# Performance work log

Measured on AMD Instinct MI355X. Metric: run time of the kernel, lower is better.

Reference implementation:

```python
import math
import jax, jax.numpy as jnp
import numpy as np

DIM = 1024
HEADS = 16
KV_HEADS = 4            # use_mqa: heads // 4
HEAD_DIM = DIM // HEADS  # 64
KV_DIM = KV_HEADS * HEAD_DIM  # 256
WINDOW = 64
SCALE = HEAD_DIM ** -0.5


def _alibi_slopes(n_heads: int) -> np.ndarray:
    # n_heads is a power of 2 here
    start = 2.0 ** (-(2.0 ** (-(math.log2(n_heads) - 3))))
    return np.array([start * (start ** i) for i in range(n_heads)], dtype=np.float32)


def setup_inputs() -> dict:
    key = jax.random.key(0)
    ks = jax.random.split(key, 5)
    B, N = 1, 2048
    x = jax.random.normal(ks[0], (B, N, DIM), dtype=jnp.float32)
    # Linear weights stored as [in, out] (applied as x @ W)
    sq = 1.0 / math.sqrt(DIM)
    Wq = jax.random.uniform(ks[1], (DIM, DIM), jnp.float32, -sq, sq)
    Wk = jax.random.uniform(ks[2], (DIM, KV_DIM), jnp.float32, -sq, sq)
    Wv = jax.random.uniform(ks[3], (DIM, KV_DIM), jnp.float32, -sq, sq)
    Wo = jax.random.uniform(ks[4], (DIM, DIM), jnp.float32, -sq, sq)
    return {"x": x, "Wq": Wq, "Wk": Wk, "Wv": Wv, "Wo": Wo}


def reference(x, Wq, Wk, Wv, Wo):
    B, N, C = x.shape
    # projections -> [B, H, N, hd]
    q = (x @ Wq).reshape(B, N, HEADS, HEAD_DIM).transpose(0, 2, 1, 3)
    k = (x @ Wk).reshape(B, N, KV_HEADS, HEAD_DIM).transpose(0, 2, 1, 3)
    v = (x @ Wv).reshape(B, N, KV_HEADS, HEAD_DIM).transpose(0, 2, 1, 3)
    # MQA: repeat kv heads (torch repeat_interleave on head dim)
    rep = HEADS // KV_HEADS
    k = jnp.repeat(k, rep, axis=1)
    v = jnp.repeat(v, rep, axis=1)

    scores = jnp.einsum("bhqd,bhkd->bhqk", q, k) * SCALE  # [B,H,N,N]

    # ALiBi bias: distance[i, j] = j - i, scaled per head
    idx = jnp.arange(N)
    dist = (idx[None, :] - idx[:, None]).astype(scores.dtype)  # [N, N]
    slopes = jnp.asarray(_alibi_slopes(HEADS))                 # [H]
    scores = scores + dist[None, None, :, :] * slopes[None, :, None, None]

    # causal AND local band (|i-j| <= WINDOW) -> allowed iff j in [i-WINDOW, i]
    causal = idx[None, :] <= idx[:, None]
    band = jnp.abs(idx[:, None] - idx[None, :]) <= WINDOW
    allowed = causal & band  # [N, N]
    scores_local = jnp.where(allowed[None, None], scores, -jnp.inf)
    attn_local = jax.nn.softmax(scores_local, axis=-1)
    out_local = jnp.einsum("bhqk,bhkd->bhqd", attn_local, v)

    # global: strided keys every WINDOW positions, full (non-causal) softmax
    k_g = k[:, :, ::WINDOW, :]
    v_g = v[:, :, ::WINDOW, :]
    scores_g = jnp.einsum("bhqd,bhkd->bhqk", q, k_g) * SCALE
    attn_g = jax.nn.softmax(scores_g, axis=-1)
    out_global = jnp.einsum("bhqk,bhkd->bhqd", attn_g, v_g)

    out = (out_local + out_global).transpose(0, 2, 1, 3).reshape(B, N, C)
    return out @ Wo
```

## Files before the change

kernel.cpp:

```cpp
#include <hip/hip_runtime.h>

#define SCALE 0.125f

typedef unsigned short ushort_t;
typedef unsigned short ushortx8 __attribute__((ext_vector_type(8)));
typedef unsigned short ushortx4 __attribute__((ext_vector_type(4)));
typedef short bf16x8 __attribute__((ext_vector_type(8)));
typedef float f32x4 __attribute__((ext_vector_type(4)));

__device__ inline ushort_t f2bf(float f) {
  unsigned int u = __float_as_uint(f);
  u += 0x7FFFu + ((u >> 16) & 1u);
  return (ushort_t)(u >> 16);
}
__device__ inline float bf2f(ushort_t u) {
  return __uint_as_float(((unsigned int)u) << 16);
}

__global__ __launch_bounds__(256) void prep_kernel(
    const float* __restrict__ x, const float* __restrict__ Wq, const float* __restrict__ Wk,
    const float* __restrict__ Wv, const float* __restrict__ Wo,
    ushort_t* __restrict__ x_bf, ushort_t* __restrict__ wqkv_t, ushort_t* __restrict__ wo_t)
{
  __shared__ float t[64][65];
  int bid = blockIdx.x;
  const int tid = threadIdx.x;
  if (bid < 2048) {
    int idx = (bid * 256 + tid) * 4;
    if (idx < 2048 * 1024) {
      float4 f = *(const float4*)(x + idx);
      ushortx4 o = { f2bf(f.x), f2bf(f.y), f2bf(f.z), f2bf(f.w) };
      *(ushortx4*)(x_bf + idx) = o;
    }
    return;
  }
  bid -= 2048;
  const float* src; int C; ushort_t* dst; int row_off, cb, kb;
  if (bid < 256)      { src = Wq; C = 1024; dst = wqkv_t; row_off = 0;    cb = bid & 15; kb = bid >> 4; }
  else if (bid < 320) { int j = bid - 256; src = Wk; C = 256; dst = wqkv_t; row_off = 1024; cb = j & 3; kb = j >> 2; }
  else if (bid < 384) { int j = bid - 320; src = Wv; C = 256; dst = wqkv_t; row_off = 1280; cb = j & 3; kb = j >> 2; }
  else                { int j = bid - 384; src = Wo; C = 1024; dst = wo_t; row_off = 0;    cb = j & 15; kb = j >> 4; }
  const int c0 = cb * 64, k0 = kb * 64;
  const int c = tid & 63, r4 = tid >> 6;
  for (int rr = r4; rr < 64; rr += 4)
    t[c][rr] = src[(size_t)(k0 + rr) * C + c0 + c];
  __syncthreads();
  const int kk = tid & 63, n4 = tid >> 6;
  for (int nn = n4; nn < 64; nn += 4)
    dst[(size_t)(row_off + c0 + nn) * 1024 + k0 + kk] = f2bf(t[nn][kk]);
}

__global__ __launch_bounds__(256) void gemm128_kernel(
    const ushort_t* __restrict__ A, const ushort_t* __restrict__ Bt, int mode, int ntn,
    ushort_t* __restrict__ qout, ushort_t* __restrict__ kout, ushort_t* __restrict__ vout,
    float* __restrict__ fout)
{
  __shared__ __align__(16) ushort_t lA[64 * 128];
  __shared__ __align__(16) ushort_t lB[64 * 128];
  const int bid = blockIdx.x;
  const int xcd = bid & 7, g = bid >> 3;
  const int m0 = (xcd + 8 * (g / ntn)) * 64;
  const int n0 = (g % ntn) * 64;

  const int tid = threadIdx.x;
  const int lane = tid & 63, w = tid >> 6;
  const int quad = lane >> 4, l16 = lane & 15;
  const int rw = (w >> 1) * 32, cw = (w & 1) * 32;

  const int rs = tid >> 4;
  const int ps = tid & 15;
  const int swz = ps ^ (rs & 15);
  const int eL = tid * 8;
  const ushort_t* Ab = A + (size_t)(m0 + rs) * 1024 + swz * 8;
  const ushort_t* Bb = Bt + (size_t)(n0 + rs) * 1024 + swz * 8;

  f32x4 acc[2][2] = {};

  for (int k0 = 0; k0 < 1024; k0 += 128) {
    __syncthreads();
#pragma unroll
    for (int rd = 0; rd < 4; ++rd) {
      __builtin_amdgcn_global_load_lds(
          (const __attribute__((address_space(1))) unsigned int*)(Ab + (size_t)rd * 16 * 1024 + k0),
          (__attribute__((address_space(3))) unsigned int*)(lA + eL + rd * 2048), 16, 0, 0);
      __builtin_amdgcn_global_load_lds(
          (const __attribute__((address_space(1))) unsigned int*)(Bb + (size_t)rd * 16 * 1024 + k0),
          (__attribute__((address_space(3))) unsigned int*)(lB + eL + rd * 2048), 16, 0, 0);
    }
    __syncthreads();

#pragma unroll
    for (int kh = 0; kh < 4; ++kh) {
      const int ca = ((kh * 4 + quad) ^ l16) << 3;
      bf16x8 a0 = *(const bf16x8*)(lA + (rw + l16) * 128      + ca);
      bf16x8 a1 = *(const bf16x8*)(lA + (rw + 16 + l16) * 128 + ca);
      bf16x8 b0 = *(const bf16x8*)(lB + (cw + l16) * 128      + ca);
      bf16x8 b1 = *(const bf16x8*)(lB + (cw + 16 + l16) * 128 + ca);
      acc[0][0] = __builtin_amdgcn_mfma_f32_16x16x32_bf16(a0, b0, acc[0][0], 0, 0, 0);
      acc[0][1] = __builtin_amdgcn_mfma_f32_16x16x32_bf16(a0, b1, acc[0][1], 0, 0, 0);
      acc[1][0] = __builtin_amdgcn_mfma_f32_16x16x32_bf16(a1, b0, acc[1][0], 0, 0, 0);
      acc[1][1] = __builtin_amdgcn_mfma_f32_16x16x32_bf16(a1, b1, acc[1][1], 0, 0, 0);
    }
  }

#pragma unroll
  for (int mg = 0; mg < 2; ++mg)
#pragma unroll
    for (int ng = 0; ng < 2; ++ng)
#pragma unroll
      for (int r = 0; r < 4; ++r) {
        const int row = m0 + rw + mg * 16 + quad * 4 + r;
        const int col = n0 + cw + ng * 16 + l16;
        const float v = acc[mg][ng][r];
        if (mode == 0) {
          if (n0 < 1024)       qout[(size_t)row * 1024 + col] = f2bf(v);
          else if (n0 < 1280)  kout[(size_t)row * 256 + (col - 1024)] = f2bf(v);
          else                 vout[(size_t)row * 256 + (col - 1280)] = f2bf(v);
        } else {
          fout[(size_t)row * 1024 + col] = v;
        }
      }
}

__global__ __launch_bounds__(256) void attn_mfma_kernel(
    const ushort_t* __restrict__ Q, const ushort_t* __restrict__ Kb,
    const ushort_t* __restrict__ Vb, ushort_t* __restrict__ O)
{
  __shared__ __align__(16) ushort_t lK[128 * 64];
  __shared__ __align__(16) ushort_t lVt[64 * 128];
  __shared__ __align__(16) ushort_t lKg[32 * 64];
  __shared__ __align__(16) ushort_t lVtg[64 * 40];
  __shared__ __align__(16) ushort_t lP[64 * 128];
  __shared__ __align__(16) ushort_t lPg[64 * 40];

  const int h = blockIdx.x, qb = blockIdx.y;
  const int tid = threadIdx.x;
  const int kvcol = (h >> 2) * 64;
  const int kbase = qb * 64 - 64;

  for (int cidx = tid; cidx < 1024; cidx += 256) {
    const int key = cidx >> 3, ch = cidx & 7;
    const int kpos = kbase + key;
    ushortx8 kv = {0,0,0,0,0,0,0,0}, vv = {0,0,0,0,0,0,0,0};
    if (kpos >= 0) {
      kv = *(const ushortx8*)(Kb + (size_t)kpos * 256 + kvcol + ch * 8);
      vv = *(const ushortx8*)(Vb + (size_t)kpos * 256 + kvcol + ch * 8);
    }
    *(ushortx8*)(lK + key * 64 + ((ch ^ (key & 7)) << 3)) = kv;
    const int kc = key >> 3, ke = key & 7;
#pragma unroll
    for (int e = 0; e < 8; ++e) {
      int dim = ch * 8 + e;
      lVt[dim * 128 + ((kc ^ (dim & 7)) << 3) + ke] = vv[e];
    }
  }
  {
    const int gk = tid >> 3, ch = tid & 7;
    const int kpos = gk * 64;
    ushortx8 kv = *(const ushortx8*)(Kb + (size_t)kpos * 256 + kvcol + ch * 8);
    ushortx8 vv = *(const ushortx8*)(Vb + (size_t)kpos * 256 + kvcol + ch * 8);
    *(ushortx8*)(lKg + gk * 64 + ((ch ^ (gk & 7)) << 3)) = kv;
#pragma unroll
    for (int e = 0; e < 8; ++e) lVtg[(ch * 8 + e) * 40 + gk] = vv[e];
  }
  __syncthreads();

  const int lane = tid & 63, w = tid >> 6;
  const int quad = lane >> 4, l16 = lane & 15;
  const int l7 = l16 & 7;
  const float slope = exp2f(-0.5f * (float)(h + 1));

  const int qrow = qb * 64 + w * 16 + l16;
  const ushort_t* qptr = Q + (size_t)qrow * 1024 + h * 64 + quad * 8;
  const bf16x8 aq0 = *(const bf16x8*)(qptr);
  const bf16x8 aq1 = *(const bf16x8*)(qptr + 32);

  float s[8][4];
#pragma unroll
  for (int kt = 0; kt < 8; ++kt) {
    const int key = kt * 16 + l16;
    const bf16x8 b0 = *(const bf16x8*)(lK + key * 64 + ((quad ^ l7) << 3));
    const bf16x8 b1 = *(const bf16x8*)(lK + key * 64 + (((4 + quad) ^ l7) << 3));
    f32x4 acc = {0.f, 0.f, 0.f, 0.f};
    acc = __builtin_amdgcn_mfma_f32_16x16x32_bf16(aq0, b0, acc, 0, 0, 0);
    acc = __builtin_amdgcn_mfma_f32_16x16x32_bf16(aq1, b1, acc, 0, 0, 0);
    const int kpos = kbase + key;
#pragma unroll
    for (int r = 0; r < 4; ++r) {
      const int qp = qb * 64 + w * 16 + quad * 4 + r;
      const int d = kpos - qp;
      const bool ok = (d <= 0) && (d >= -64) && (kpos >= 0);
      s[kt][r] = ok ? acc[r] * SCALE + (float)d * slope : -1e30f;
    }
  }
  float mr[4] = {-1e30f, -1e30f, -1e30f, -1e30f};
#pragma unroll
  for (int kt = 0; kt < 8; ++kt)
#pragma unroll
    for (int r = 0; r < 4; ++r) mr[r] = fmaxf(mr[r], s[kt][r]);
#pragma unroll
  for (int r = 0; r < 4; ++r) {
    mr[r] = fmaxf(mr[r], __shfl_xor(mr[r], 1));
    mr[r] = fmaxf(mr[r], __shfl_xor(mr[r], 2));
    mr[r] = fmaxf(mr[r], __shfl_xor(mr[r], 4));
    mr[r] = fmaxf(mr[r], __shfl_xor(mr[r], 8));
  }
  float lr[4] = {0.f, 0.f, 0.f, 0.f};
#pragma unroll
  for (int kt = 0; kt < 8; ++kt)
#pragma unroll
    for (int r = 0; r < 4; ++r) { float p = __expf(s[kt][r] - mr[r]); s[kt][r] = p; lr[r] += p; }
#pragma unroll
  for (int r = 0; r < 4; ++r) {
    lr[r] += __shfl_xor(lr[r], 1);
    lr[r] += __shfl_xor(lr[r], 2);
    lr[r] += __shfl_xor(lr[r], 4);
    lr[r] += __shfl_xor(lr[r], 8);
    lr[r] = 1.f / lr[r];
  }
#pragma unroll
  for (int kt = 0; kt < 8; ++kt) {
    const int kc = kt * 2 + (l16 >> 3);
#pragma unroll
    for (int r = 0; r < 4; ++r) {
      const int qr = w * 16 + quad * 4 + r;
      lP[qr * 128 + ((kc ^ (qr & 7)) << 3) + l7] = f2bf(s[kt][r] * lr[r]);
    }
  }

  float sg[2][4];
#pragma unroll
  for (int g16 = 0; g16 < 2; ++g16) {
    const int key = g16 * 16 + l16;
    const bf16x8 b0 = *(const bf16x8*)(lKg + key * 64 + ((quad ^ l7) << 3));
    const bf16x8 b1 = *(const bf16x8*)(lKg + key * 64 + (((4 + quad) ^ l7) << 3));
    f32x4 acc = {0.f, 0.f, 0.f, 0.f};
    acc = __builtin_amdgcn_mfma_f32_16x16x32_bf16(aq0, b0, acc, 0, 0, 0);
    acc = __builtin_amdgcn_mfma_f32_16x16x32_bf16(aq1, b1, acc, 0, 0, 0);
#pragma unroll
    for (int r = 0; r < 4; ++r) sg[g16][r] = acc[r] * SCALE;
  }
  float mg[4], lg[4];
#pragma unroll
  for (int r = 0; r < 4; ++r) {
    mg[r] = fmaxf(sg[0][r], sg[1][r]);
    mg[r] = fmaxf(mg[r], __shfl_xor(mg[r], 1));
    mg[r] = fmaxf(mg[r], __shfl_xor(mg[r], 2));
    mg[r] = fmaxf(mg[r], __shfl_xor(mg[r], 4));
    mg[r] = fmaxf(mg[r], __shfl_xor(mg[r], 8));
  }
#pragma unroll
  for (int r = 0; r < 4; ++r) {
    float p0 = __expf(sg[0][r] - mg[r]);
    float p1 = __expf(sg[1][r] - mg[r]);
    sg[0][r] = p0; sg[1][r] = p1;
    lg[r] = p0 + p1;
    lg[r] += __shfl_xor(lg[r], 1);
    lg[r] += __shfl_xor(lg[r], 2);
    lg[r] += __shfl_xor(lg[r], 4);
    lg[r] += __shfl_xor(lg[r], 8);
    lg[r] = 1.f / lg[r];
  }
#pragma unroll
  for (int g16 = 0; g16 < 2; ++g16)
#pragma unroll
    for (int r = 0; r < 4; ++r) {
      const int qr = w * 16 + quad * 4 + r;
      lPg[qr * 40 + g16 * 16 + l16] = f2bf(sg[g16][r] * lg[r]);
    }

  f32x4 acco[4] = {};
  const int qA = w * 16 + l16;
#pragma unroll
  for (int kki = 0; kki < 4; ++kki) {
    const bf16x8 ap = *(const bf16x8*)(lP + qA * 128 + (((kki * 4 + quad) ^ l7) << 3));
#pragma unroll
    for (int nt = 0; nt < 4; ++nt) {
      const int dim = nt * 16 + l16;
      const bf16x8 bv = *(const bf16x8*)(lVt + dim * 128 + (((kki * 4 + quad) ^ l7) << 3));
      acco[nt] = __builtin_amdgcn_mfma_f32_16x16x32_bf16(ap, bv, acco[nt], 0, 0, 0);
    }
  }
  {
    const bf16x8 apg = *(const bf16x8*)(lPg + qA * 40 + quad * 8);
#pragma unroll
    for (int nt = 0; nt < 4; ++nt) {
      const bf16x8 bvg = *(const bf16x8*)(lVtg + (nt * 16 + l16) * 40 + quad * 8);
      acco[nt] = __builtin_amdgcn_mfma_f32_16x16x32_bf16(apg, bvg, acco[nt], 0, 0, 0);
    }
  }
#pragma unroll
  for (int nt = 0; nt < 4; ++nt)
#pragma unroll
    for (int r = 0; r < 4; ++r) {
      const int qp = qb * 64 + w * 16 + quad * 4 + r;
      O[(size_t)qp * 1024 + h * 64 + nt * 16 + l16] = f2bf(acco[nt][r]);
    }
}

extern "C" void kernel_launch(void* const* d_in, const int* in_sizes, int n_in,
                              void* d_out, int out_size, void* d_ws, size_t ws_size,
                              hipStream_t stream)
{
  const float* x  = (const float*)d_in[0];
  const float* Wq = (const float*)d_in[1];
  const float* Wk = (const float*)d_in[2];
  const float* Wv = (const float*)d_in[3];
  const float* Wo = (const float*)d_in[4];
  float* out = (float*)d_out;

  char* ws = (char*)d_ws;
  ushort_t* x_bf   = (ushort_t*)(ws);
  ushort_t* wqkv_t = (ushort_t*)(ws + (4ull  << 20));
  ushort_t* wo_t   = (ushort_t*)(ws + (7ull  << 20));
  ushort_t* q_bf   = (ushort_t*)(ws + (9ull  << 20));
  ushort_t* k_bf   = (ushort_t*)(ws + (13ull << 20));
  ushort_t* v_bf   = (ushort_t*)(ws + (14ull << 20));
  ushort_t* at_bf  = (ushort_t*)(ws + (15ull << 20));

  prep_kernel<<<2688, 256, 0, stream>>>(x, Wq, Wk, Wv, Wo, x_bf, wqkv_t, wo_t);
  gemm128_kernel<<<768, 256, 0, stream>>>(x_bf, wqkv_t, 0, 24, q_bf, k_bf, v_bf, nullptr);
  attn_mfma_kernel<<<dim3(16, 32), 256, 0, stream>>>(q_bf, k_bf, v_bf, at_bf);
  gemm128_kernel<<<512, 256, 0, stream>>>(at_bf, wo_t, 1, 16, nullptr, nullptr, nullptr, out);
}
```

Before: 106.6 us.

## Make GEMMs persistent with double-buffered LDS prefetch across output tiles

Replaces the one-tile-per-block GEMM with a persistent kernel of 256 blocks, where each block walks several 64x64 output tiles sharing the same A rows. LDS is double-buffered so the next k-slice (or the next tile's first slice) is issued via global_load_lds before computing the current one, removing one barrier per step. Launch overhead and tail waves go down and the A-tile stays hot in cache. The cost is fewer concurrent blocks (256 against the CU count), less latency hiding from occupancy, and twice the LDS per block.

```diff
diff --git a/kernel.cpp b/kernel.cpp
--- a/kernel.cpp
+++ b/kernel.cpp
@@ -50,76 +50,91 @@
     dst[(size_t)(row_off + c0 + nn) * 1024 + k0 + kk] = f2bf(t[nn][kk]);
 }
 
-__global__ __launch_bounds__(256) void gemm128_kernel(
-    const ushort_t* __restrict__ A, const ushort_t* __restrict__ Bt, int mode, int ntn,
+__global__ __launch_bounds__(256) void gemm_pers_kernel(
+    const ushort_t* __restrict__ A, const ushort_t* __restrict__ Bt, int mode, int tpb,
     ushort_t* __restrict__ qout, ushort_t* __restrict__ kout, ushort_t* __restrict__ vout,
     float* __restrict__ fout)
 {
-  __shared__ __align__(16) ushort_t lA[64 * 128];
-  __shared__ __align__(16) ushort_t lB[64 * 128];
+  __shared__ __align__(16) ushort_t lA[2 * 64 * 128];
+  __shared__ __align__(16) ushort_t lB[2 * 64 * 128];
   const int bid = blockIdx.x;
-  const int xcd = bid & 7, g = bid >> 3;
-  const int m0 = (xcd + 8 * (g / ntn)) * 64;
-  const int n0 = (g % ntn) * 64;
+  const int xcd = bid & 7, idx = bid >> 3;
+  const int m0 = (xcd * 4 + (idx & 3)) * 64;
+  const int n_base = idx >> 2;
 
   const int tid = threadIdx.x;
   const int lane = tid & 63, w = tid >> 6;
   const int quad = lane >> 4, l16 = lane & 15;
   const int rw = (w >> 1) * 32, cw = (w & 1) * 32;
 
-  const int rs = tid >> 4;
-  const int ps = tid & 15;
+  const int rs = tid >> 4, ps = tid & 15;
   const int swz = ps ^ (rs & 15);
   const int eL = tid * 8;
   const ushort_t* Ab = A + (size_t)(m0 + rs) * 1024 + swz * 8;
-  const ushort_t* Bb = Bt + (size_t)(n0 + rs) * 1024 + swz * 8;
-
+  const ushort_t* Bb0 = Bt + (size_t)(n_base * 64 + rs) * 1024 + swz * 8;
+
+  const int NS = tpb * 8;
   f32x4 acc[2][2] = {};
 
-  for (int k0 = 0; k0 < 1024; k0 += 128) {
+#define STAGE(s, b)                                                                             \
+  do {                                                                                          \
+    const int j_ = (s) >> 3, k0_ = ((s) & 7) * 128;                                             \
+    const ushort_t* Bb_ = Bb0 + (size_t)j_ * 512 * 1024;                                        \
+    const int off_ = (b) * 8192;                                                                \
+    _Pragma("unroll")                                                                           \
+    for (int rd = 0; rd < 4; ++rd) {                                                            \
+      __builtin_amdgcn_global_load_lds(                                                         \
+          (const __attribute__((address_space(1))) unsigned int*)(Ab + (size_t)rd * 16 * 1024 + k0_), \
+          (__attribute__((address_space(3))) unsigned int*)(lA + off_ + eL + rd * 2048), 16, 0, 0);   \
+      __builtin_amdgcn_global_load_lds(                                                         \
+          (const __attribute__((address_space(1))) unsigned int*)(Bb_ + (size_t)rd * 16 * 1024 + k0_), \
+          (__attribute__((address_space(3))) unsigned int*)(lB + off_ + eL + rd * 2048), 16, 0, 0);   \
+    }                                                                                           \
+  } while (0)
+
+  STAGE(0, 0);
+
+  for (int s = 0; s < NS; ++s) {
+    const int b = s & 1;
     __syncthreads();
-#pragma unroll
-    for (int rd = 0; rd < 4; ++rd) {
-      __builtin_amdgcn_global_load_lds(
-          (const __attribute__((address_space(1))) unsigned int*)(Ab + (size_t)rd * 16 * 1024 + k0),
-          (__attribute__((address_space(3))) unsigned int*)(lA + eL + rd * 2048), 16, 0, 0);
-      __builtin_amdgcn_global_load_lds(
-          (const __attribute__((address_space(1))) unsigned int*)(Bb + (size_t)rd * 16 * 1024 + k0),
-          (__attribute__((address_space(3))) unsigned int*)(lB + eL + rd * 2048), 16, 0, 0);
-    }
-    __syncthreads();
-
+    if (s + 1 < NS) STAGE(s + 1, b ^ 1);
+    const int off = b * 8192;
 #pragma unroll
     for (int kh = 0; kh < 4; ++kh) {
       const int ca = ((kh * 4 + quad) ^ l16) << 3;
-      bf16x8 a0 = *(const bf16x8*)(lA + (rw + l16) * 128      + ca);
-      bf16x8 a1 = *(const bf16x8*)(lA + (rw + 16 + l16) * 128 + ca);
-      bf16x8 b0 = *(const bf16x8*)(lB + (cw + l16) * 128      + ca);
-      bf16x8 b1 = *(const bf16x8*)(lB + (cw + 16 + l16) * 128 + ca);
+      bf16x8 a0 = *(const bf16x8*)(lA + off + (rw + l16) * 128      + ca);
+      bf16x8 a1 = *(const bf16x8*)(lA + off + (rw + 16 + l16) * 128 + ca);
+      bf16x8 b0 = *(const bf16x8*)(lB + off + (cw + l16) * 128      + ca);
+      bf16x8 b1 = *(const bf16x8*)(lB + off + (cw + 16 + l16) * 128 + ca);
       acc[0][0] = __builtin_amdgcn_mfma_f32_16x16x32_bf16(a0, b0, acc[0][0], 0, 0, 0);
       acc[0][1] = __builtin_amdgcn_mfma_f32_16x16x32_bf16(a0, b1, acc[0][1], 0, 0, 0);
       acc[1][0] = __builtin_amdgcn_mfma_f32_16x16x32_bf16(a1, b0, acc[1][0], 0, 0, 0);
       acc[1][1] = __builtin_amdgcn_mfma_f32_16x16x32_bf16(a1, b1, acc[1][1], 0, 0, 0);
     }
-  }
-
-#pragma unroll
-  for (int mg = 0; mg < 2; ++mg)
-#pragma unroll
-    for (int ng = 0; ng < 2; ++ng)
-#pragma unroll
-      for (int r = 0; r < 4; ++r) {
-        const int row = m0 + rw + mg * 16 + quad * 4 + r;
-        const int col = n0 + cw + ng * 16 + l16;
-        const float v = acc[mg][ng][r];
-        if (mode == 0) {
-          if (n0 < 1024)       qout[(size_t)row * 1024 + col] = f2bf(v);
-          else if (n0 < 1280)  kout[(size_t)row * 256 + (col - 1024)] = f2bf(v);
-          else                 vout[(size_t)row * 256 + (col - 1280)] = f2bf(v);
-        } else {
-          fout[(size_t)row * 1024 + col] = v;
+    if ((s & 7) == 7) {
+      const int n0 = (n_base + 8 * (s >> 3)) * 64;
+#pragma unroll
+      for (int mg = 0; mg < 2; ++mg)
+#pragma unroll
+        for (int ng = 0; ng < 2; ++ng) {
+#pragma unroll
+          for (int r = 0; r < 4; ++r) {
+            const int row = m0 + rw + mg * 16 + quad * 4 + r;
+            const int col = n0 + cw + ng * 16 + l16;
+            const float v = acc[mg][ng][r];
+            if (mode == 0) {
+              if (n0 < 1024)       qout[(size_t)row * 1024 + col] = f2bf(v);
+              else if (n0 < 1280)  kout[(size_t)row * 256 + (col - 1024)] = f2bf(v);
+              else                 vout[(size_t)row * 256 + (col - 1280)] = f2bf(v);
+            } else {
+              fout[(size_t)row * 1024 + col] = v;
+            }
+          }
+          acc[mg][ng] = (f32x4){0.f, 0.f, 0.f, 0.f};
         }
-      }
+    }
+  }
+#undef STAGE
 }
 
 __global__ __launch_bounds__(256) void attn_mfma_kernel(
@@ -319,7 +334,7 @@
   ushort_t* at_bf  = (ushort_t*)(ws + (15ull << 20));
 
   prep_kernel<<<2688, 256, 0, stream>>>(x, Wq, Wk, Wv, Wo, x_bf, wqkv_t, wo_t);
-  gemm128_kernel<<<768, 256, 0, stream>>>(x_bf, wqkv_t, 0, 24, q_bf, k_bf, v_bf, nullptr);
+  gemm_pers_kernel<<<256, 256, 0, stream>>>(x_bf, wqkv_t, 0, 3, q_bf, k_bf, v_bf, nullptr);
   attn_mfma_kernel<<<dim3(16, 32), 256, 0, stream>>>(q_bf, k_bf, v_bf, at_bf);
-  gemm128_kernel<<<512, 256, 0, stream>>>(at_bf, wo_t, 1, 16, nullptr, nullptr, nullptr, out);
-}
+  gemm_pers_kernel<<<256, 256, 0, stream>>>(at_bf, wo_t, 1, 2, nullptr, nullptr, nullptr, out);
+}
```

After: 129.3 us. 1.21x slower.

## Split GEMM K dimension in two with atomic fp32 accumulation

Applied to the files above, without the earlier changes.

Both projection GEMMs now split the 1024-long K loop into two halves run by separate blocks, which doubles the grid, and combine partial sums with fp32 atomicAdd into zeroed buffers. Q/K/V are therefore kept in fp32, and the attention kernel converts them to bf16 on load. The aim is more parallelism and occupancy for small GEMMs. In exchange it adds two memsets, doubles the intermediate traffic for the fp32 Q/K/V, and adds atomic contention.

```diff
diff --git a/kernel.cpp b/kernel.cpp
--- a/kernel.cpp
+++ b/kernel.cpp
@@ -50,25 +50,27 @@
     dst[(size_t)(row_off + c0 + nn) * 1024 + k0 + kk] = f2bf(t[nn][kk]);
 }
 
-__global__ __launch_bounds__(256) void gemm128_kernel(
-    const ushort_t* __restrict__ A, const ushort_t* __restrict__ Bt, int mode, int ntn,
-    ushort_t* __restrict__ qout, ushort_t* __restrict__ kout, ushort_t* __restrict__ vout,
+__global__ __launch_bounds__(256, 5) void gemm_sk2_kernel(
+    const ushort_t* __restrict__ A, const ushort_t* __restrict__ Bt, int ntile, int ntn, int mode,
+    float* __restrict__ qf, float* __restrict__ kf, float* __restrict__ vf,
     float* __restrict__ fout)
 {
   __shared__ __align__(16) ushort_t lA[64 * 128];
   __shared__ __align__(16) ushort_t lB[64 * 128];
-  const int bid = blockIdx.x;
+  int bid = blockIdx.x;
+  const int kh = bid >= ntile ? 1 : 0;
+  bid -= kh * ntile;
   const int xcd = bid & 7, g = bid >> 3;
   const int m0 = (xcd + 8 * (g / ntn)) * 64;
   const int n0 = (g % ntn) * 64;
+  const int ks = kh * 512;
 
   const int tid = threadIdx.x;
   const int lane = tid & 63, w = tid >> 6;
   const int quad = lane >> 4, l16 = lane & 15;
   const int rw = (w >> 1) * 32, cw = (w & 1) * 32;
 
-  const int rs = tid >> 4;
-  const int ps = tid & 15;
+  const int rs = tid >> 4, ps = tid & 15;
   const int swz = ps ^ (rs & 15);
   const int eL = tid * 8;
   const ushort_t* Ab = A + (size_t)(m0 + rs) * 1024 + swz * 8;
@@ -76,7 +78,7 @@
 
   f32x4 acc[2][2] = {};
 
-  for (int k0 = 0; k0 < 1024; k0 += 128) {
+  for (int k0 = ks; k0 < ks + 512; k0 += 128) {
     __syncthreads();
 #pragma unroll
     for (int rd = 0; rd < 4; ++rd) {
@@ -90,8 +92,8 @@
     __syncthreads();
 
 #pragma unroll
-    for (int kh = 0; kh < 4; ++kh) {
-      const int ca = ((kh * 4 + quad) ^ l16) << 3;
+    for (int khh = 0; khh < 4; ++khh) {
+      const int ca = ((khh * 4 + quad) ^ l16) << 3;
       bf16x8 a0 = *(const bf16x8*)(lA + (rw + l16) * 128      + ca);
       bf16x8 a1 = *(const bf16x8*)(lA + (rw + 16 + l16) * 128 + ca);
       bf16x8 b0 = *(const bf16x8*)(lB + (cw + l16) * 128      + ca);
@@ -113,18 +115,18 @@
         const int col = n0 + cw + ng * 16 + l16;
         const float v = acc[mg][ng][r];
         if (mode == 0) {
-          if (n0 < 1024)       qout[(size_t)row * 1024 + col] = f2bf(v);
-          else if (n0 < 1280)  kout[(size_t)row * 256 + (col - 1024)] = f2bf(v);
-          else                 vout[(size_t)row * 256 + (col - 1280)] = f2bf(v);
+          if (col < 1024)      atomicAdd(qf + (size_t)row * 1024 + col, v);
+          else if (col < 1280) atomicAdd(kf + (size_t)row * 256 + (col - 1024), v);
+          else                 atomicAdd(vf + (size_t)row * 256 + (col - 1280), v);
         } else {
-          fout[(size_t)row * 1024 + col] = v;
+          atomicAdd(fout + (size_t)row * 1024 + col, v);
         }
       }
 }
 
 __global__ __launch_bounds__(256) void attn_mfma_kernel(
-    const ushort_t* __restrict__ Q, const ushort_t* __restrict__ Kb,
-    const ushort_t* __restrict__ Vb, ushort_t* __restrict__ O)
+    const float* __restrict__ Qf, const float* __restrict__ Kf,
+    const float* __restrict__ Vf, ushort_t* __restrict__ O)
 {
   __shared__ __align__(16) ushort_t lK[128 * 64];
   __shared__ __align__(16) ushort_t lVt[64 * 128];
@@ -143,8 +145,14 @@
     const int kpos = kbase + key;
     ushortx8 kv = {0,0,0,0,0,0,0,0}, vv = {0,0,0,0,0,0,0,0};
     if (kpos >= 0) {
-      kv = *(const ushortx8*)(Kb + (size_t)kpos * 256 + kvcol + ch * 8);
-      vv = *(const ushortx8*)(Vb + (size_t)kpos * 256 + kvcol + ch * 8);
+      const float* kr = Kf + (size_t)kpos * 256 + kvcol + ch * 8;
+      const float* vr = Vf + (size_t)kpos * 256 + kvcol + ch * 8;
+      float4 k0 = *(const float4*)(kr), k1 = *(const float4*)(kr + 4);
+      float4 v0 = *(const float4*)(vr), v1 = *(const float4*)(vr + 4);
+      kv[0]=f2bf(k0.x); kv[1]=f2bf(k0.y); kv[2]=f2bf(k0.z); kv[3]=f2bf(k0.w);
+      kv[4]=f2bf(k1.x); kv[5]=f2bf(k1.y); kv[6]=f2bf(k1.z); kv[7]=f2bf(k1.w);
+      vv[0]=f2bf(v0.x); vv[1]=f2bf(v0.y); vv[2]=f2bf(v0.z); vv[3]=f2bf(v0.w);
+      vv[4]=f2bf(v1.x); vv[5]=f2bf(v1.y); vv[6]=f2bf(v1.z); vv[7]=f2bf(v1.w);
     }
     *(ushortx8*)(lK + key * 64 + ((ch ^ (key & 7)) << 3)) = kv;
     const int kc = key >> 3, ke = key & 7;
@@ -157,8 +165,15 @@
   {
     const int gk = tid >> 3, ch = tid & 7;
     const int kpos = gk * 64;
-    ushortx8 kv = *(const ushortx8*)(Kb + (size_t)kpos * 256 + kvcol + ch * 8);
-    ushortx8 vv = *(const ushortx8*)(Vb + (size_t)kpos * 256 + kvcol + ch * 8);
+    const float* kr = Kf + (size_t)kpos * 256 + kvcol + ch * 8;
+    const float* vr = Vf + (size_t)kpos * 256 + kvcol + ch * 8;
+    float4 k0 = *(const float4*)(kr), k1 = *(const float4*)(kr + 4);
+    float4 v0 = *(const float4*)(vr), v1 = *(const float4*)(vr + 4);
+    ushortx8 kv, vv;
+    kv[0]=f2bf(k0.x); kv[1]=f2bf(k0.y); kv[2]=f2bf(k0.z); kv[3]=f2bf(k0.w);
+    kv[4]=f2bf(k1.x); kv[5]=f2bf(k1.y); kv[6]=f2bf(k1.z); kv[7]=f2bf(k1.w);
+    vv[0]=f2bf(v0.x); vv[1]=f2bf(v0.y); vv[2]=f2bf(v0.z); vv[3]=f2bf(v0.w);
+    vv[4]=f2bf(v1.x); vv[5]=f2bf(v1.y); vv[6]=f2bf(v1.z); vv[7]=f2bf(v1.w);
     *(ushortx8*)(lKg + gk * 64 + ((ch ^ (gk & 7)) << 3)) = kv;
 #pragma unroll
     for (int e = 0; e < 8; ++e) lVtg[(ch * 8 + e) * 40 + gk] = vv[e];
@@ -171,9 +186,16 @@
   const float slope = exp2f(-0.5f * (float)(h + 1));
 
   const int qrow = qb * 64 + w * 16 + l16;
-  const ushort_t* qptr = Q + (size_t)qrow * 1024 + h * 64 + quad * 8;
-  const bf16x8 aq0 = *(const bf16x8*)(qptr);
-  const bf16x8 aq1 = *(const bf16x8*)(qptr + 32);
+  bf16x8 aq0, aq1;
+  {
+    const float* qp = Qf + (size_t)qrow * 1024 + h * 64 + quad * 8;
+    float4 a = *(const float4*)(qp), b = *(const float4*)(qp + 4);
+    float4 c = *(const float4*)(qp + 32), d = *(const float4*)(qp + 36);
+    aq0[0]=f2bf(a.x); aq0[1]=f2bf(a.y); aq0[2]=f2bf(a.z); aq0[3]=f2bf(a.w);
+    aq0[4]=f2bf(b.x); aq0[5]=f2bf(b.y); aq0[6]=f2bf(b.z); aq0[7]=f2bf(b.w);
+    aq1[0]=f2bf(c.x); aq1[1]=f2bf(c.y); aq1[2]=f2bf(c.z); aq1[3]=f2bf(c.w);
+    aq1[4]=f2bf(d.x); aq1[5]=f2bf(d.y); aq1[6]=f2bf(d.z); aq1[7]=f2bf(d.w);
+  }
 
   float s[8][4];
 #pragma unroll
@@ -313,13 +335,16 @@
   ushort_t* x_bf   = (ushort_t*)(ws);
   ushort_t* wqkv_t = (ushort_t*)(ws + (4ull  << 20));
   ushort_t* wo_t   = (ushort_t*)(ws + (7ull  << 20));
-  ushort_t* q_bf   = (ushort_t*)(ws + (9ull  << 20));
-  ushort_t* k_bf   = (ushort_t*)(ws + (13ull << 20));
-  ushort_t* v_bf   = (ushort_t*)(ws + (14ull << 20));
-  ushort_t* at_bf  = (ushort_t*)(ws + (15ull << 20));
+  float*    qf     = (float*)(ws + (9ull  << 20));
+  float*    kf     = (float*)(ws + (17ull << 20));
+  float*    vf     = (float*)(ws + (19ull << 20));
+  ushort_t* at_bf  = (ushort_t*)(ws + (21ull << 20));
+
+  hipMemsetAsync(qf, 0, 12ull << 20, stream);
+  hipMemsetAsync(out, 0, (size_t)out_size * sizeof(float), stream);
 
   prep_kernel<<<2688, 256, 0, stream>>>(x, Wq, Wk, Wv, Wo, x_bf, wqkv_t, wo_t);
-  gemm128_kernel<<<768, 256, 0, stream>>>(x_bf, wqkv_t, 0, 24, q_bf, k_bf, v_bf, nullptr);
-  attn_mfma_kernel<<<dim3(16, 32), 256, 0, stream>>>(q_bf, k_bf, v_bf, at_bf);
-  gemm128_kernel<<<512, 256, 0, stream>>>(at_bf, wo_t, 1, 16, nullptr, nullptr, nullptr, out);
-}
+  gemm_sk2_kernel<<<1536, 256, 0, stream>>>(x_bf, wqkv_t, 768, 24, 0, qf, kf, vf, nullptr);
+  attn_mfma_kernel<<<dim3(16, 32), 256, 0, stream>>>(qf, kf, vf, at_bf);
+  gemm_sk2_kernel<<<1024, 256, 0, stream>>>(at_bf, wo_t, 512, 16, 1, nullptr, nullptr, nullptr, out);
+}
```

After: 136.9 us. 28.4% more time.

## Double-buffer GEMM K-tiles through registers to overlap global loads with MFMA

Applied to the files above, without the earlier changes.

Replaces the single-buffered 128-wide K-tile GEMM, which used direct global-to-LDS loads, with a register-staged double-buffered pipeline over 64-wide K-tiles. The next tile is loaded into registers while MFMAs run on the current LDS buffer, then written to the alternate buffer, so each iteration needs one barrier instead of two. An XOR swizzle over 8 chunks is kept, and launch bounds now request 4 blocks per CU. The trade-offs are twice as many loop iterations and extra register pressure from holding the staged data.

```diff
diff --git a/kernel.cpp b/kernel.cpp
--- a/kernel.cpp
+++ b/kernel.cpp
@@ -50,13 +50,13 @@
     dst[(size_t)(row_off + c0 + nn) * 1024 + k0 + kk] = f2bf(t[nn][kk]);
 }
 
-__global__ __launch_bounds__(256) void gemm128_kernel(
+__global__ __launch_bounds__(256, 4) void gemm_pipe_kernel(
     const ushort_t* __restrict__ A, const ushort_t* __restrict__ Bt, int mode, int ntn,
     ushort_t* __restrict__ qout, ushort_t* __restrict__ kout, ushort_t* __restrict__ vout,
     float* __restrict__ fout)
 {
-  __shared__ __align__(16) ushort_t lA[64 * 128];
-  __shared__ __align__(16) ushort_t lB[64 * 128];
+  __shared__ __align__(16) ushort_t lA[2 * 64 * 64];
+  __shared__ __align__(16) ushort_t lB[2 * 64 * 64];
   const int bid = blockIdx.x;
   const int xcd = bid & 7, g = bid >> 3;
   const int m0 = (xcd + 8 * (g / ntn)) * 64;
@@ -66,41 +66,58 @@
   const int lane = tid & 63, w = tid >> 6;
   const int quad = lane >> 4, l16 = lane & 15;
   const int rw = (w >> 1) * 32, cw = (w & 1) * 32;
-
-  const int rs = tid >> 4;
-  const int ps = tid & 15;
-  const int swz = ps ^ (rs & 15);
-  const int eL = tid * 8;
-  const ushort_t* Ab = A + (size_t)(m0 + rs) * 1024 + swz * 8;
-  const ushort_t* Bb = Bt + (size_t)(n0 + rs) * 1024 + swz * 8;
+  const int l7 = l16 & 7;
+
+  const int srow = tid >> 2;
+  const int c0 = (tid & 3) * 2;
+  const int r7s = srow & 7;
+  const ushort_t* Ag = A + (size_t)(m0 + srow) * 1024 + c0 * 8;
+  const ushort_t* Bg = Bt + (size_t)(n0 + srow) * 1024 + c0 * 8;
+  const int wO0 = srow * 64 + ((c0 ^ r7s) << 3);
+  const int wO1 = srow * 64 + (((c0 + 1) ^ r7s) << 3);
 
   f32x4 acc[2][2] = {};
-
-  for (int k0 = 0; k0 < 1024; k0 += 128) {
-    __syncthreads();
-#pragma unroll
-    for (int rd = 0; rd < 4; ++rd) {
-      __builtin_amdgcn_global_load_lds(
-          (const __attribute__((address_space(1))) unsigned int*)(Ab + (size_t)rd * 16 * 1024 + k0),
-          (__attribute__((address_space(3))) unsigned int*)(lA + eL + rd * 2048), 16, 0, 0);
-      __builtin_amdgcn_global_load_lds(
-          (const __attribute__((address_space(1))) unsigned int*)(Bb + (size_t)rd * 16 * 1024 + k0),
-          (__attribute__((address_space(3))) unsigned int*)(lB + eL + rd * 2048), 16, 0, 0);
-    }
-    __syncthreads();
-
-#pragma unroll
-    for (int kh = 0; kh < 4; ++kh) {
-      const int ca = ((kh * 4 + quad) ^ l16) << 3;
-      bf16x8 a0 = *(const bf16x8*)(lA + (rw + l16) * 128      + ca);
-      bf16x8 a1 = *(const bf16x8*)(lA + (rw + 16 + l16) * 128 + ca);
-      bf16x8 b0 = *(const bf16x8*)(lB + (cw + l16) * 128      + ca);
-      bf16x8 b1 = *(const bf16x8*)(lB + (cw + 16 + l16) * 128 + ca);
+  bf16x8 ra0, ra1, rb0, rb1;
+
+  ra0 = *(const bf16x8*)(Ag);
+  ra1 = *(const bf16x8*)(Ag + 8);
+  rb0 = *(const bf16x8*)(Bg);
+  rb1 = *(const bf16x8*)(Bg + 8);
+  *(bf16x8*)(lA + wO0) = ra0;
+  *(bf16x8*)(lA + wO1) = ra1;
+  *(bf16x8*)(lB + wO0) = rb0;
+  *(bf16x8*)(lB + wO1) = rb1;
+  __syncthreads();
+
+  for (int it = 0; it < 16; ++it) {
+    const int cur = (it & 1) * 4096;
+    const int nxt = 4096 - cur;
+    if (it < 15) {
+      const int k0 = (it + 1) * 64;
+      ra0 = *(const bf16x8*)(Ag + k0);
+      ra1 = *(const bf16x8*)(Ag + k0 + 8);
+      rb0 = *(const bf16x8*)(Bg + k0);
+      rb1 = *(const bf16x8*)(Bg + k0 + 8);
+    }
+#pragma unroll
+    for (int kh = 0; kh < 2; ++kh) {
+      const int ca = ((kh * 4 + quad) ^ l7) << 3;
+      bf16x8 a0 = *(const bf16x8*)(lA + cur + (rw + l16) * 64      + ca);
+      bf16x8 a1 = *(const bf16x8*)(lA + cur + (rw + 16 + l16) * 64 + ca);
+      bf16x8 b0 = *(const bf16x8*)(lB + cur + (cw + l16) * 64      + ca);
+      bf16x8 b1 = *(const bf16x8*)(lB + cur + (cw + 16 + l16) * 64 + ca);
       acc[0][0] = __builtin_amdgcn_mfma_f32_16x16x32_bf16(a0, b0, acc[0][0], 0, 0, 0);
       acc[0][1] = __builtin_amdgcn_mfma_f32_16x16x32_bf16(a0, b1, acc[0][1], 0, 0, 0);
       acc[1][0] = __builtin_amdgcn_mfma_f32_16x16x32_bf16(a1, b0, acc[1][0], 0, 0, 0);
       acc[1][1] = __builtin_amdgcn_mfma_f32_16x16x32_bf16(a1, b1, acc[1][1], 0, 0, 0);
     }
+    if (it < 15) {
+      *(bf16x8*)(lA + nxt + wO0) = ra0;
+      *(bf16x8*)(lA + nxt + wO1) = ra1;
+      *(bf16x8*)(lB + nxt + wO0) = rb0;
+      *(bf16x8*)(lB + nxt + wO1) = rb1;
+    }
+    __syncthreads();
   }
 
 #pragma unroll
@@ -319,7 +336,7 @@
   ushort_t* at_bf  = (ushort_t*)(ws + (15ull << 20));
 
   prep_kernel<<<2688, 256, 0, stream>>>(x, Wq, Wk, Wv, Wo, x_bf, wqkv_t, wo_t);
-  gemm128_kernel<<<768, 256, 0, stream>>>(x_bf, wqkv_t, 0, 24, q_bf, k_bf, v_bf, nullptr);
+  gemm_pipe_kernel<<<768, 256, 0, stream>>>(x_bf, wqkv_t, 0, 24, q_bf, k_bf, v_bf, nullptr);
   attn_mfma_kernel<<<dim3(16, 32), 256, 0, stream>>>(q_bf, k_bf, v_bf, at_bf);
-  gemm128_kernel<<<512, 256, 0, stream>>>(at_bf, wo_t, 1, 16, nullptr, nullptr, nullptr, out);
-}
+  gemm_pipe_kernel<<<512, 256, 0, stream>>>(at_bf, wo_t, 1, 16, nullptr, nullptr, nullptr, out);
+}
```

Result: slower. 109.8 us (+3.1%).
